# Kernel optimization log

Hardware: AMD Instinct MI355X
Metric: run time of the kernel (lower is better)

The kernel has to match this reference:

```python
import jax, jax.numpy as jnp
import numpy as np

D_MODEL = 1024
N_HEADS = 16
D_K = D_MODEL // N_HEADS
NEG = -1e9


def setup_inputs() -> dict:
    key = jax.random.key(0)
    ks = jax.random.split(key, 6)
    B, T, D = 4, 2048, D_MODEL
    s = 1.0 / np.sqrt(D)
    x = jax.random.normal(ks[0], (B, T, D), dtype=jnp.float32)
    Wq = jax.random.normal(ks[1], (D, D), dtype=jnp.float32) * s
    Wk = jax.random.normal(ks[2], (D, D), dtype=jnp.float32) * s
    Wv = jax.random.normal(ks[3], (D, D), dtype=jnp.float32) * s
    Wo = jax.random.normal(ks[4], (D, D), dtype=jnp.float32) * s
    bo = jnp.zeros((D,), dtype=jnp.float32)
    # causal mask: True above diagonal = masked (masked_fill where True)
    mask = jnp.triu(jnp.ones((T, T), dtype=bool), k=1)
    return {"x": x, "mask": mask, "Wq": Wq, "Wk": Wk, "Wv": Wv, "Wo": Wo, "bo": bo}


def reference(x, mask, Wq, Wk, Wv, Wo, bo):
    B, T, D = x.shape
    # torch nn.Linear: y = x @ W.T
    q = (x @ Wq.T).reshape(B, T, N_HEADS, D_K).transpose(0, 2, 1, 3)  # [B,H,T,dk]
    k = (x @ Wk.T).reshape(B, T, N_HEADS, D_K).transpose(0, 2, 1, 3)
    v = (x @ Wv.T).reshape(B, T, N_HEADS, D_K).transpose(0, 2, 1, 3)
    scores = jnp.einsum("bhqd,bhkd->bhqk", q, k) / np.sqrt(D_K)  # [B,H,T,T]
    scores = jnp.where(mask[:T, :T], NEG, scores)
    attn = jax.nn.softmax(scores, axis=-1)
    ctx = jnp.einsum("bhqk,bhkd->bhqd", attn, v)  # [B,H,T,dk]
    ctx = ctx.transpose(0, 2, 1, 3).reshape(B, T, D)
    return ctx @ Wo.T + bo
```

## Files before the change

### kernel.cpp

```cpp
#include <hip/hip_runtime.h>
#include <hip/hip_bf16.h>


typedef __attribute__((ext_vector_type(8))) short bf16x8;
typedef __attribute__((ext_vector_type(4))) float f32x4;

__device__ __forceinline__ unsigned short f2b(float x) {
  __hip_bfloat16 h = __float2bfloat16(x);
  return __builtin_bit_cast(unsigned short, h);
}

__device__ __forceinline__ void load_lds16(const void* g, void* l) {
  __builtin_amdgcn_global_load_lds((__attribute__((address_space(1))) void*)g,
                                   (__attribute__((address_space(3))) void*)l,
                                   16, 0, 0);
}

__global__ void cast_kernel(const float* __restrict__ x,
                            const float* __restrict__ w0, const float* __restrict__ w1,
                            const float* __restrict__ w2, const float* __restrict__ w3,
                            unsigned short* __restrict__ xb, unsigned short* __restrict__ wb) {
  int i = blockIdx.x * 256 + threadIdx.x;
  const float* src;
  unsigned short* dst;
  int c;
  if (i < 1048576) {
    src = x; dst = xb; c = i;
  } else {
    int cw = i - 1048576;
    int wi = cw >> 17;
    c = cw & 131071;
    src = (wi == 0) ? w0 : (wi == 1) ? w1 : (wi == 2) ? w2 : w3;
    dst = wb + ((size_t)wi << 20);
  }
  const float4* s4 = (const float4*)src;
  float4 a = s4[2 * c], b = s4[2 * c + 1];
  union { unsigned short u[8]; uint4 v; } r;
  r.u[0] = f2b(a.x); r.u[1] = f2b(a.y); r.u[2] = f2b(a.z); r.u[3] = f2b(a.w);
  r.u[4] = f2b(b.x); r.u[5] = f2b(b.y); r.u[6] = f2b(b.z); r.u[7] = f2b(b.w);
  ((uint4*)dst)[c] = r.v;
}

__launch_bounds__(512, 2)
__global__ void gemm_qkv(const unsigned short* __restrict__ A,
                         const unsigned short* __restrict__ Bw,
                         unsigned short* __restrict__ Cout) {
  __shared__ unsigned short At[3][256 * 64];
  __shared__ unsigned short Bt[3][128 * 64];

  const int tid = threadIdx.x;
  const int lane = tid & 63;
  const int w = tid >> 6;
  const int quad = lane >> 4;
  const int l15 = lane & 15;
  const int m0 = blockIdx.x * 256;
  const int n0 = blockIdx.y * 128;
  const int wm = (w & 3) * 64;
  const int wn = (w >> 2) * 64;

  auto stageA = [&](int buf, int kt, int c) {
    int chunk = c * 512 + tid;
    int row = chunk >> 3;
    int scol = (chunk & 7) ^ (row & 7);
    load_lds16(A + (size_t)(m0 + row) * 1024 + kt + scol * 8,
               &At[buf][(c * 512 + (w << 6)) << 3]);
  };
  auto stageB = [&](int buf, int kt, int c) {
    int chunk = c * 512 + tid;
    int row = chunk >> 3;
    int scol = (chunk & 7) ^ (row & 7);
    load_lds16(Bw + (size_t)(n0 + row) * 1024 + kt + scol * 8,
               &Bt[buf][(c * 512 + (w << 6)) << 3]);
  };

  const f32x4 z4 = {0.f, 0.f, 0.f, 0.f};
  f32x4 acc[4][4];
#pragma unroll
  for (int i = 0; i < 4; ++i)
#pragma unroll
    for (int j = 0; j < 4; ++j) acc[i][j] = z4;

#pragma unroll
  for (int c = 0; c < 4; ++c) stageA(0, 0, c);
#pragma unroll
  for (int c = 0; c < 2; ++c) stageB(0, 0, c);
#pragma unroll
  for (int c = 0; c < 4; ++c) stageA(1, 64, c);
#pragma unroll
  for (int c = 0; c < 2; ++c) stageB(1, 64, c);
  asm volatile("s_waitcnt vmcnt(6)" ::: "memory");
  __builtin_amdgcn_s_barrier();
  __builtin_amdgcn_sched_barrier(0);

  int buf = 0;
  for (int t = 0; t < 16; ++t) {
    const int sbuf = (buf >= 1) ? buf - 1 : 2;
    const int skt = (t + 2) * 64;
    const bool st = (t < 14);

    bf16x8 bfv[4][2];
    bf16x8 afv[2][2];

#pragma unroll
    for (int j = 0; j < 4; ++j) {
      int rowB = wn + j * 16 + l15;
#pragma unroll
      for (int ks = 0; ks < 2; ++ks)
        bfv[j][ks] = *(const bf16x8*)&Bt[buf][rowB * 64 + (((ks * 4 + quad) ^ (rowB & 7)) << 3)];
    }
#pragma unroll
    for (int ii = 0; ii < 2; ++ii) {
      int rowA = wm + ii * 16 + l15;
#pragma unroll
      for (int ks = 0; ks < 2; ++ks)
        afv[ii][ks] = *(const bf16x8*)&At[buf][rowA * 64 + (((ks * 4 + quad) ^ (rowA & 7)) << 3)];
    }
    if (st) { stageA(sbuf, skt, 0); stageA(sbuf, skt, 1); stageB(sbuf, skt, 0); }
    __builtin_amdgcn_s_barrier();
    __builtin_amdgcn_sched_barrier(0);
    __builtin_amdgcn_s_setprio(1);
#pragma unroll
    for (int ii = 0; ii < 2; ++ii)
#pragma unroll
      for (int j = 0; j < 4; ++j)
#pragma unroll
        for (int ks = 0; ks < 2; ++ks)
          acc[ii][j] = __builtin_amdgcn_mfma_f32_16x16x32_bf16(afv[ii][ks], bfv[j][ks],
                                                               acc[ii][j], 0, 0, 0);
    __builtin_amdgcn_s_setprio(0);
    __builtin_amdgcn_s_barrier();
    __builtin_amdgcn_sched_barrier(0);

#pragma unroll
    for (int ii = 0; ii < 2; ++ii) {
      int rowA = wm + 32 + ii * 16 + l15;
#pragma unroll
      for (int ks = 0; ks < 2; ++ks)
        afv[ii][ks] = *(const bf16x8*)&At[buf][rowA * 64 + (((ks * 4 + quad) ^ (rowA & 7)) << 3)];
    }
    if (st) { stageA(sbuf, skt, 2); stageA(sbuf, skt, 3); stageB(sbuf, skt, 1); }
    __builtin_amdgcn_s_barrier();
    __builtin_amdgcn_sched_barrier(0);
    __builtin_amdgcn_s_setprio(1);
#pragma unroll
    for (int ii = 0; ii < 2; ++ii)
#pragma unroll
      for (int j = 0; j < 4; ++j)
#pragma unroll
        for (int ks = 0; ks < 2; ++ks)
          acc[2 + ii][j] = __builtin_amdgcn_mfma_f32_16x16x32_bf16(afv[ii][ks], bfv[j][ks],
                                                                   acc[2 + ii][j], 0, 0, 0);
    __builtin_amdgcn_s_setprio(0);

    if (t < 14) {
      asm volatile("s_waitcnt vmcnt(6)" ::: "memory");
    } else if (t == 14) {
      asm volatile("s_waitcnt vmcnt(0)" ::: "memory");
    }
    __builtin_amdgcn_s_barrier();
    __builtin_amdgcn_sched_barrier(0);

    buf = (buf < 2) ? buf + 1 : 0;
  }

  const int seg = n0 >> 10;
#pragma unroll
  for (int i = 0; i < 4; ++i) {
#pragma unroll
    for (int j = 0; j < 4; ++j) {
#pragma unroll
      for (int r = 0; r < 4; ++r) {
        int m = m0 + wm + i * 16 + quad * 4 + r;
        int n = n0 + wn + j * 16 + l15;
        int nn = n & 1023;
        float v = acc[i][j][r];
        if (seg == 0) {
          Cout[(size_t)m * 1024 + nn] = f2b(v);
        } else if (seg == 1) {
          (Cout + 8388608)[(size_t)m * 1024 + nn] = f2b(v);
        } else {
          int b = m >> 11, tq = m & 2047, hh = nn >> 6, d = nn & 63;
          (Cout + 16777216)[(((size_t)((b * 16 + hh) * 64 + d)) << 11) + tq] = f2b(v);
        }
      }
    }
  }
}

__launch_bounds__(256)
__global__ void gemm_proj(const unsigned short* __restrict__ A,
                          const unsigned short* __restrict__ Bw,
                          const float* __restrict__ bias,
                          float* __restrict__ out) {
  __shared__ unsigned short At[128 * 64];
  __shared__ unsigned short Bt[64 * 64];

  const int tid = threadIdx.x;
  const int lane = tid & 63;
  const int w = tid >> 6;
  const int quad = lane >> 4;
  const int l15 = lane & 15;
  const int m0 = blockIdx.x * 128;
  const int n0 = blockIdx.y * 64;
  const int wm = w * 32;

  const f32x4 z4 = {0.f, 0.f, 0.f, 0.f};
  f32x4 acc[2][4];
#pragma unroll
  for (int i = 0; i < 2; ++i)
#pragma unroll
    for (int j = 0; j < 4; ++j) acc[i][j] = z4;

  for (int kt = 0; kt < 1024; kt += 64) {
    __syncthreads();
#pragma unroll
    for (int c = 0; c < 4; ++c) {
      int chunk = c * 256 + tid;
      int row = chunk >> 3;
      int scol = (chunk & 7) ^ (row & 7);
      load_lds16(A + (size_t)(m0 + row) * 1024 + kt + scol * 8,
                 &At[((c * 256 + (w << 6)) << 3)]);
    }
#pragma unroll
    for (int c = 0; c < 2; ++c) {
      int chunk = c * 256 + tid;
      int row = chunk >> 3;
      int scol = (chunk & 7) ^ (row & 7);
      load_lds16(Bw + (size_t)(n0 + row) * 1024 + kt + scol * 8,
                 &Bt[((c * 256 + (w << 6)) << 3)]);
    }
    __syncthreads();
#pragma unroll
    for (int ks = 0; ks < 2; ++ks) {
      bf16x8 af[2], bf[4];
#pragma unroll
      for (int i = 0; i < 2; ++i) {
        int rowA = wm + i * 16 + l15;
        af[i] = *(const bf16x8*)&At[rowA * 64 + (((ks * 4 + quad) ^ (rowA & 7)) << 3)];
      }
#pragma unroll
      for (int j = 0; j < 4; ++j) {
        int rowB = j * 16 + l15;
        bf[j] = *(const bf16x8*)&Bt[rowB * 64 + (((ks * 4 + quad) ^ (rowB & 7)) << 3)];
      }
#pragma unroll
      for (int i = 0; i < 2; ++i)
#pragma unroll
        for (int j = 0; j < 4; ++j)
          acc[i][j] = __builtin_amdgcn_mfma_f32_16x16x32_bf16(af[i], bf[j], acc[i][j], 0, 0, 0);
    }
  }

#pragma unroll
  for (int i = 0; i < 2; ++i)
#pragma unroll
    for (int j = 0; j < 4; ++j) {
      int n = n0 + j * 16 + l15;
      float bv = bias[n];
#pragma unroll
      for (int r = 0; r < 4; ++r) {
        int m = m0 + wm + i * 16 + quad * 4 + r;
        out[(size_t)m * 1024 + n] = acc[i][j][r] + bv;
      }
    }
}

__launch_bounds__(256)
__global__ void attn_kernel(const unsigned short* __restrict__ Q,
                            const unsigned short* __restrict__ K,
                            const unsigned short* __restrict__ VT,
                            unsigned short* __restrict__ ctx) {
  __shared__ unsigned short Kt[2][64 * 64];
  __shared__ unsigned short Vt[2][64 * 64];
  __shared__ unsigned short Pt[128 * 64];

  const int tid = threadIdx.x;
  const int lane = tid & 63;
  const int w = tid >> 6;
  const int quad = lane >> 4;
  const int l15 = lane & 15;
  const int bh = blockIdx.x;
  const int pp = blockIdx.y;
  const int b = bh >> 4, h = bh & 15;

  const unsigned short* Kg = K + ((size_t)(b * 2048)) * 1024 + h * 64;
  const unsigned short* Vg = VT + ((size_t)bh * 64) * 2048;

  const float SC = 0.1803368801f;
  const float M0 = 11.0f;

  for (int tt = 0; tt < 2; ++tt) {
    const int qt = tt ? (15 - pp) : pp;
    const int qb = qt * 128;
    const int jn = 2 * qt + 2;

    bf16x8 qa[2][2];
#pragma unroll
    for (int g = 0; g < 2; ++g) {
      const unsigned short* qbase =
          Q + ((size_t)(b * 2048 + qb + w * 32 + g * 16 + l15)) * 1024 + h * 64;
      qa[g][0] = *(const bf16x8*)(qbase + quad * 8);
      qa[g][1] = *(const bf16x8*)(qbase + 32 + quad * 8);
    }

    const f32x4 z4 = {0.f, 0.f, 0.f, 0.f};
    f32x4 o[2][4];
#pragma unroll
    for (int g = 0; g < 2; ++g)
#pragma unroll
      for (int nt = 0; nt < 4; ++nt) o[g][nt] = z4;
    float lrow[2] = {0.f, 0.f};

    if (tt) __syncthreads();

#pragma unroll
    for (int c = 0; c < 2; ++c) {
      int chunk = c * 256 + tid;
      int row = chunk >> 3;
      int scol = (chunk & 7) ^ (row & 7);
      load_lds16(Kg + (size_t)row * 1024 + scol * 8, &Kt[0][((c * 256 + (w << 6)) << 3)]);
      load_lds16(Vg + ((size_t)row << 11) + scol * 8, &Vt[0][((c * 256 + (w << 6)) << 3)]);
    }

    int cur = 0;
    for (int j = 0; j < jn; ++j) {
      const int j0 = j * 64;
      __syncthreads();

      if (j + 1 < jn) {
        const int nj0 = j0 + 64;
#pragma unroll
        for (int c = 0; c < 2; ++c) {
          int chunk = c * 256 + tid;
          int row = chunk >> 3;
          int scol = (chunk & 7) ^ (row & 7);
          load_lds16(Kg + (size_t)(nj0 + row) * 1024 + scol * 8,
                     &Kt[cur ^ 1][((c * 256 + (w << 6)) << 3)]);
          load_lds16(Vg + ((size_t)row << 11) + nj0 + scol * 8,
                     &Vt[cur ^ 1][((c * 256 + (w << 6)) << 3)]);
        }
      }

      f32x4 st[2][4];
#pragma unroll
      for (int g = 0; g < 2; ++g)
#pragma unroll
        for (int nt = 0; nt < 4; ++nt) st[g][nt] = z4;
#pragma unroll
      for (int ks = 0; ks < 2; ++ks) {
#pragma unroll
        for (int nt = 0; nt < 4; ++nt) {
          int rowK = nt * 16 + l15;
          bf16x8 kf = *(const bf16x8*)&Kt[cur][rowK * 64 + (((ks * 4 + quad) ^ (rowK & 7)) << 3)];
          st[0][nt] = __builtin_amdgcn_mfma_f32_16x16x32_bf16(kf, qa[0][ks], st[0][nt], 0, 0, 0);
          st[1][nt] = __builtin_amdgcn_mfma_f32_16x16x32_bf16(kf, qa[1][ks], st[1][nt], 0, 0, 0);
        }
      }

#pragma unroll
      for (int g = 0; g < 2; ++g) {
        const int qmin = qb + w * 32 + g * 16;
        const bool dg = (j0 + 63 > qmin);
        const int q = qmin + l15;
        float sum = 0.f;
#pragma unroll
        for (int nt = 0; nt < 4; ++nt) {
#pragma unroll
          for (int r = 0; r < 4; ++r) {
            float e = fmaf(st[g][nt][r], SC, -M0);
            if (dg) {
              int kpos = j0 + nt * 16 + quad * 4 + r;
              if (kpos > q) e = -1e30f;
            }
            float pv = __builtin_amdgcn_exp2f(e);
            st[g][nt][r] = pv;
            sum += pv;
          }
        }
        sum += __shfl_xor(sum, 16);
        sum += __shfl_xor(sum, 32);
        lrow[g] += sum;
      }

#pragma unroll
      for (int g = 0; g < 2; ++g) {
        const int qrow = w * 32 + g * 16 + l15;
#pragma unroll
        for (int nt = 0; nt < 4; ++nt) {
          ushort4 pk;
          pk.x = f2b(st[g][nt][0]); pk.y = f2b(st[g][nt][1]);
          pk.z = f2b(st[g][nt][2]); pk.w = f2b(st[g][nt][3]);
          int chunk = nt * 4 + quad;
          *(ushort4*)&Pt[qrow * 64 + ((chunk ^ l15) << 2)] = pk;
        }
      }

#pragma unroll
      for (int ks = 0; ks < 2; ++ks) {
        int c0 = ks * 8 + quad * 2;
        union { ushort4 hh[2]; bf16x8 v; } pu[2];
#pragma unroll
        for (int g = 0; g < 2; ++g) {
          const int qrow = w * 32 + g * 16 + l15;
          pu[g].hh[0] = *(const ushort4*)&Pt[qrow * 64 + ((c0 ^ l15) << 2)];
          pu[g].hh[1] = *(const ushort4*)&Pt[qrow * 64 + (((c0 + 1) ^ l15) << 2)];
        }
#pragma unroll
        for (int nt = 0; nt < 4; ++nt) {
          int rowV = nt * 16 + l15;
          bf16x8 vb = *(const bf16x8*)&Vt[cur][rowV * 64 + (((ks * 4 + quad) ^ (rowV & 7)) << 3)];
          o[0][nt] = __builtin_amdgcn_mfma_f32_16x16x32_bf16(pu[0].v, vb, o[0][nt], 0, 0, 0);
          o[1][nt] = __builtin_amdgcn_mfma_f32_16x16x32_bf16(pu[1].v, vb, o[1][nt], 0, 0, 0);
        }
      }
      cur ^= 1;
    }

#pragma unroll
    for (int g = 0; g < 2; ++g) {
      float lf[4];
#pragma unroll
      for (int r = 0; r < 4; ++r) lf[r] = 1.f / __shfl(lrow[g], quad * 4 + r);
#pragma unroll
      for (int nt = 0; nt < 4; ++nt) {
#pragma unroll
        for (int r = 0; r < 4; ++r) {
          int q = qb + w * 32 + g * 16 + quad * 4 + r;
          int dcol = nt * 16 + l15;
          ctx[((size_t)(b * 2048 + q)) * 1024 + h * 64 + dcol] = f2b(o[g][nt][r] * lf[r]);
        }
      }
    }
  }
}

extern "C" void kernel_launch(void* const* d_in, const int* in_sizes, int n_in,
                              void* d_out, int out_size, void* d_ws, size_t ws_size,
                              hipStream_t stream) {
  const float* x  = (const float*)d_in[0];
  const float* Wq = (const float*)d_in[2];
  const float* Wk = (const float*)d_in[3];
  const float* Wv = (const float*)d_in[4];
  const float* Wo = (const float*)d_in[5];
  const float* bo = (const float*)d_in[6];
  float* out = (float*)d_out;

  unsigned short* xb  = (unsigned short*)d_ws;
  unsigned short* wb  = xb + 8388608;
  unsigned short* Qb  = wb + 4 * 1048576;
  unsigned short* Kb  = Qb + 8388608;
  unsigned short* VTb = Kb + 8388608;
  unsigned short* ctxb = xb;

  cast_kernel<<<6144, 256, 0, stream>>>(x, Wq, Wk, Wv, Wo, xb, wb);

  gemm_qkv<<<dim3(32, 24), 512, 0, stream>>>(xb, wb, Qb);

  attn_kernel<<<dim3(64, 8), 256, 0, stream>>>(Qb, Kb, VTb, ctxb);

  gemm_proj<<<dim3(64, 16), 256, 0, stream>>>(ctxb, wb + 3 * 1048576, bo, out);
}
```

Measured before the change: 278.7 us.

## Enlarge QKV GEMM tile to 256x256 with double-buffered LDS

The fused QKV projection GEMM tile grows from 256x128 to 256x256, so each wave computes a 128x64 sub-tile with 32 accumulators, and the grid halves to 32x12 blocks. The LDS pipeline changes from triple buffering of 256x64/128x64 tiles to double buffering of two 256x64 tiles, with the A and B stages issued in different phases and a full vmcnt(0) wait per K step. This aims to raise arithmetic intensity and cut global/LDS traffic per FLOP, but it increases register pressure, shrinks the prefetch depth, and leaves fewer blocks (384) to fill the CUs.

```diff
diff --git a/kernel.cpp b/kernel.cpp
--- a/kernel.cpp
+++ b/kernel.cpp
@@ -45,8 +45,8 @@
 __global__ void gemm_qkv(const unsigned short* __restrict__ A,
                          const unsigned short* __restrict__ Bw,
                          unsigned short* __restrict__ Cout) {
-  __shared__ unsigned short At[3][256 * 64];
-  __shared__ unsigned short Bt[3][128 * 64];
+  __shared__ unsigned short At[2][256 * 64];
+  __shared__ unsigned short Bt[2][256 * 64];
 
   const int tid = threadIdx.x;
   const int lane = tid & 63;
@@ -54,118 +54,136 @@
   const int quad = lane >> 4;
   const int l15 = lane & 15;
   const int m0 = blockIdx.x * 256;
-  const int n0 = blockIdx.y * 128;
-  const int wm = (w & 3) * 64;
-  const int wn = (w >> 2) * 64;
-
-  auto stageA = [&](int buf, int kt, int c) {
+  const int n0 = blockIdx.y * 256;
+  const int wm = (w >> 2) * 128;
+  const int wn = (w & 3) * 64;
+
+  auto stage = [&](const unsigned short* G, unsigned short* L, int kt, int c) {
     int chunk = c * 512 + tid;
     int row = chunk >> 3;
     int scol = (chunk & 7) ^ (row & 7);
-    load_lds16(A + (size_t)(m0 + row) * 1024 + kt + scol * 8,
-               &At[buf][(c * 512 + (w << 6)) << 3]);
+    load_lds16(G + (size_t)row * 1024 + kt + scol * 8, L + ((c * 512 + (w << 6)) << 3));
   };
-  auto stageB = [&](int buf, int kt, int c) {
-    int chunk = c * 512 + tid;
-    int row = chunk >> 3;
-    int scol = (chunk & 7) ^ (row & 7);
-    load_lds16(Bw + (size_t)(n0 + row) * 1024 + kt + scol * 8,
-               &Bt[buf][(c * 512 + (w << 6)) << 3]);
+  const unsigned short* Ag = A + (size_t)m0 * 1024;
+  const unsigned short* Bg = Bw + (size_t)n0 * 1024;
+
+  const f32x4 z4 = {0.f, 0.f, 0.f, 0.f};
+  f32x4 acc[8][4];
+#pragma unroll
+  for (int i = 0; i < 8; ++i)
+#pragma unroll
+    for (int j = 0; j < 4; ++j) acc[i][j] = z4;
+
+  auto loadA = [&](bf16x8 (&af)[4][2], int kb, int mq) {
+#pragma unroll
+    for (int i = 0; i < 4; ++i) {
+      int rowA = wm + mq * 64 + i * 16 + l15;
+#pragma unroll
+      for (int ks = 0; ks < 2; ++ks)
+        af[i][ks] = *(const bf16x8*)&At[kb][rowA * 64 + (((ks * 4 + quad) ^ (rowA & 7)) << 3)];
+    }
   };
-
-  const f32x4 z4 = {0.f, 0.f, 0.f, 0.f};
-  f32x4 acc[4][4];
-#pragma unroll
-  for (int i = 0; i < 4; ++i)
-#pragma unroll
-    for (int j = 0; j < 4; ++j) acc[i][j] = z4;
-
-#pragma unroll
-  for (int c = 0; c < 4; ++c) stageA(0, 0, c);
-#pragma unroll
-  for (int c = 0; c < 2; ++c) stageB(0, 0, c);
-#pragma unroll
-  for (int c = 0; c < 4; ++c) stageA(1, 64, c);
-#pragma unroll
-  for (int c = 0; c < 2; ++c) stageB(1, 64, c);
-  asm volatile("s_waitcnt vmcnt(6)" ::: "memory");
+  auto loadB = [&](bf16x8 (&bf)[2][2], int kb, int nq) {
+#pragma unroll
+    for (int j = 0; j < 2; ++j) {
+      int rowB = wn + nq * 32 + j * 16 + l15;
+#pragma unroll
+      for (int ks = 0; ks < 2; ++ks)
+        bf[j][ks] = *(const bf16x8*)&Bt[kb][rowB * 64 + (((ks * 4 + quad) ^ (rowB & 7)) << 3)];
+    }
+  };
+
+#pragma unroll
+  for (int c = 0; c < 4; ++c) stage(Ag, &At[0][0], 0, c);
+#pragma unroll
+  for (int c = 0; c < 4; ++c) stage(Bg, &Bt[0][0], 0, c);
+  asm volatile("s_waitcnt vmcnt(0)" ::: "memory");
   __builtin_amdgcn_s_barrier();
   __builtin_amdgcn_sched_barrier(0);
 
-  int buf = 0;
   for (int t = 0; t < 16; ++t) {
-    const int sbuf = (buf >= 1) ? buf - 1 : 2;
-    const int skt = (t + 2) * 64;
-    const bool st = (t < 14);
-
-    bf16x8 bfv[4][2];
-    bf16x8 afv[2][2];
-
-#pragma unroll
-    for (int j = 0; j < 4; ++j) {
-      int rowB = wn + j * 16 + l15;
-#pragma unroll
-      for (int ks = 0; ks < 2; ++ks)
-        bfv[j][ks] = *(const bf16x8*)&Bt[buf][rowB * 64 + (((ks * 4 + quad) ^ (rowB & 7)) << 3)];
-    }
-#pragma unroll
-    for (int ii = 0; ii < 2; ++ii) {
-      int rowA = wm + ii * 16 + l15;
-#pragma unroll
-      for (int ks = 0; ks < 2; ++ks)
-        afv[ii][ks] = *(const bf16x8*)&At[buf][rowA * 64 + (((ks * 4 + quad) ^ (rowA & 7)) << 3)];
-    }
-    if (st) { stageA(sbuf, skt, 0); stageA(sbuf, skt, 1); stageB(sbuf, skt, 0); }
+    const int kb = t & 1;
+    const int sb = kb ^ 1;
+    const int ktn = (t + 1) * 64;
+    const bool st = (t < 15);
+
+    bf16x8 af[4][2], b0[2][2], b1[2][2];
+
+    loadA(af, kb, 0);
+    loadB(b0, kb, 0);
+    if (st) {
+#pragma unroll
+      for (int c = 0; c < 4; ++c) stage(Ag, &At[sb][0], ktn, c);
+    }
     __builtin_amdgcn_s_barrier();
     __builtin_amdgcn_sched_barrier(0);
     __builtin_amdgcn_s_setprio(1);
 #pragma unroll
-    for (int ii = 0; ii < 2; ++ii)
-#pragma unroll
-      for (int j = 0; j < 4; ++j)
+    for (int i = 0; i < 4; ++i)
+#pragma unroll
+      for (int j = 0; j < 2; ++j)
 #pragma unroll
         for (int ks = 0; ks < 2; ++ks)
-          acc[ii][j] = __builtin_amdgcn_mfma_f32_16x16x32_bf16(afv[ii][ks], bfv[j][ks],
-                                                               acc[ii][j], 0, 0, 0);
+          acc[i][j] = __builtin_amdgcn_mfma_f32_16x16x32_bf16(af[i][ks], b0[j][ks],
+                                                              acc[i][j], 0, 0, 0);
     __builtin_amdgcn_s_setprio(0);
     __builtin_amdgcn_s_barrier();
     __builtin_amdgcn_sched_barrier(0);
 
-#pragma unroll
-    for (int ii = 0; ii < 2; ++ii) {
-      int rowA = wm + 32 + ii * 16 + l15;
-#pragma unroll
-      for (int ks = 0; ks < 2; ++ks)
-        afv[ii][ks] = *(const bf16x8*)&At[buf][rowA * 64 + (((ks * 4 + quad) ^ (rowA & 7)) << 3)];
-    }
-    if (st) { stageA(sbuf, skt, 2); stageA(sbuf, skt, 3); stageB(sbuf, skt, 1); }
+    loadB(b1, kb, 1);
+    if (st) {
+#pragma unroll
+      for (int c = 0; c < 4; ++c) stage(Bg, &Bt[sb][0], ktn, c);
+    }
     __builtin_amdgcn_s_barrier();
     __builtin_amdgcn_sched_barrier(0);
     __builtin_amdgcn_s_setprio(1);
 #pragma unroll
-    for (int ii = 0; ii < 2; ++ii)
-#pragma unroll
-      for (int j = 0; j < 4; ++j)
+    for (int i = 0; i < 4; ++i)
+#pragma unroll
+      for (int j = 0; j < 2; ++j)
 #pragma unroll
         for (int ks = 0; ks < 2; ++ks)
-          acc[2 + ii][j] = __builtin_amdgcn_mfma_f32_16x16x32_bf16(afv[ii][ks], bfv[j][ks],
-                                                                   acc[2 + ii][j], 0, 0, 0);
+          acc[i][2 + j] = __builtin_amdgcn_mfma_f32_16x16x32_bf16(af[i][ks], b1[j][ks],
+                                                                  acc[i][2 + j], 0, 0, 0);
     __builtin_amdgcn_s_setprio(0);
-
-    if (t < 14) {
-      asm volatile("s_waitcnt vmcnt(6)" ::: "memory");
-    } else if (t == 14) {
-      asm volatile("s_waitcnt vmcnt(0)" ::: "memory");
-    }
-    __builtin_amdgcn_s_barrier();
-    __builtin_amdgcn_sched_barrier(0);
-
-    buf = (buf < 2) ? buf + 1 : 0;
+    __builtin_amdgcn_s_barrier();
+    __builtin_amdgcn_sched_barrier(0);
+
+    loadA(af, kb, 1);
+    __builtin_amdgcn_s_barrier();
+    __builtin_amdgcn_sched_barrier(0);
+    __builtin_amdgcn_s_setprio(1);
+#pragma unroll
+    for (int i = 0; i < 4; ++i)
+#pragma unroll
+      for (int j = 0; j < 2; ++j)
+#pragma unroll
+        for (int ks = 0; ks < 2; ++ks)
+          acc[4 + i][2 + j] = __builtin_amdgcn_mfma_f32_16x16x32_bf16(af[i][ks], b1[j][ks],
+                                                                      acc[4 + i][2 + j], 0, 0, 0);
+    __builtin_amdgcn_s_setprio(0);
+    __builtin_amdgcn_s_barrier();
+    __builtin_amdgcn_sched_barrier(0);
+
+    __builtin_amdgcn_s_setprio(1);
+#pragma unroll
+    for (int i = 0; i < 4; ++i)
+#pragma unroll
+      for (int j = 0; j < 2; ++j)
+#pragma unroll
+        for (int ks = 0; ks < 2; ++ks)
+          acc[4 + i][j] = __builtin_amdgcn_mfma_f32_16x16x32_bf16(af[i][ks], b0[j][ks],
+                                                                  acc[4 + i][j], 0, 0, 0);
+    __builtin_amdgcn_s_setprio(0);
+    if (st) asm volatile("s_waitcnt vmcnt(0)" ::: "memory");
+    __builtin_amdgcn_s_barrier();
+    __builtin_amdgcn_sched_barrier(0);
   }
 
   const int seg = n0 >> 10;
 #pragma unroll
-  for (int i = 0; i < 4; ++i) {
+  for (int i = 0; i < 8; ++i) {
 #pragma unroll
     for (int j = 0; j < 4; ++j) {
 #pragma unroll
@@ -454,7 +472,7 @@
 
   cast_kernel<<<6144, 256, 0, stream>>>(x, Wq, Wk, Wv, Wo, xb, wb);
 
-  gemm_qkv<<<dim3(32, 24), 512, 0, stream>>>(xb, wb, Qb);
+  gemm_qkv<<<dim3(32, 12), 512, 0, stream>>>(xb, wb, Qb);
 
   attn_kernel<<<dim3(64, 8), 256, 0, stream>>>(Qb, Kb, VTb, ctxb);
 
```

Result: slower. 286.9 us (+2.9%).
